# Kernel tuning notes

Measured on AMD Instinct MI355X. Metric: run time of the kernel, lower is better.

## Reference

```python
import jax, jax.numpy as jnp
import numpy as np

BN_EPS = 1e-3


def _three_nn(unknown, known):
    # unknown: [B, N2, 3] query points; known: [B, N1, 3]
    # returns squared distances and indices of the 3 nearest known points
    # (CUDA three_nn returns squared euclidean distances).
    d2 = (jnp.sum(unknown * unknown, -1)[:, :, None]
          + jnp.sum(known * known, -1)[:, None, :]
          - 2.0 * jnp.einsum('bnd,bmd->bnm', unknown, known))  # [B, N2, N1]
    neg_top, ind = jax.lax.top_k(-d2, 3)                        # [B, N2, 3]
    dist2 = jnp.maximum(-neg_top, 0.0)
    return dist2, ind


def _conv_bn_relu(x, W, b, gamma, beta, mean, var):
    # x: [B, C_in, N]; W: [C_out, C_in] (1x1 conv); inference-mode BN
    y = jnp.einsum('oc,bcn->bon', W, x) + b[None, :, None]
    scale = gamma / jnp.sqrt(var + BN_EPS)
    y = (y - mean[None, :, None]) * scale[None, :, None] + beta[None, :, None]
    return jax.nn.relu(y)


def setup_inputs() -> dict:
    key = jax.random.key(0)
    ks = jax.random.split(key, 12)
    B, N1, N2, C1, C2, H = 2, 4096, 16384, 256, 128, 256
    return {
        'points1': jax.random.normal(ks[0], (B, 3, N1), jnp.float32),
        'points2': jax.random.normal(ks[1], (B, 3, N2), jnp.float32),
        'features1': jax.random.normal(ks[2], (B, C1, N1), jnp.float32),
        'features2': jax.random.normal(ks[3], (B, C2, N2), jnp.float32),
        'W1': jax.random.normal(ks[4], (H, C1 + C2), jnp.float32) * 0.05,
        'b1': jax.random.normal(ks[5], (H,), jnp.float32) * 0.05,
        'gamma1': jnp.ones((H,), jnp.float32),
        'beta1': jnp.zeros((H,), jnp.float32),
        'mean1': jax.random.normal(ks[6], (H,), jnp.float32) * 0.1,
        'var1': jax.random.uniform(ks[7], (H,), jnp.float32, 0.5, 1.5),
        'W2': jax.random.normal(ks[8], (H, H), jnp.float32) * 0.05,
        'b2': jax.random.normal(ks[9], (H,), jnp.float32) * 0.05,
        'gamma2': jnp.ones((H,), jnp.float32),
        'beta2': jnp.zeros((H,), jnp.float32),
        'mean2': jax.random.normal(ks[10], (H,), jnp.float32) * 0.1,
        'var2': jax.random.uniform(ks[11], (H,), jnp.float32, 0.5, 1.5),
    }


def reference(points1, points2, features1, features2,
              W1, b1, gamma1, beta1, mean1, var1,
              W2, b2, gamma2, beta2, mean2, var2):
    # 3-NN of each dense point (points2) among coarse points (points1)
    unknown = jnp.swapaxes(points2, 1, 2)  # [B, N2, 3]
    known = jnp.swapaxes(points1, 1, 2)    # [B, N1, 3]
    dist, ind = _three_nn(unknown, known)  # dist: squared distances [B, N2, 3]
    dist = dist * dist                     # forward squares again (as in source)
    dist = jnp.maximum(dist, 1e-10)
    inv = 1.0 / dist
    weights = inv / jnp.sum(inv, axis=2, keepdims=True)  # [B, N2, 3]

    # gather features of the 3 neighbors: features1 [B, C1, N1] -> [B, N2, 3, C1]
    f1 = jnp.swapaxes(features1, 1, 2)  # [B, N1, C1]
    gathered = jax.vmap(lambda f, i: f[i])(f1, ind)  # [B, N2, 3, C1]
    interp = jnp.einsum('bnkc,bnk->bcn', gathered, weights)  # [B, C1, N2]

    x = jnp.concatenate([interp, features2], axis=1)  # [B, C1+C2, N2]
    x = _conv_bn_relu(x, W1, b1, gamma1, beta1, mean1, var1)
    x = _conv_bn_relu(x, W2, b2, gamma2, beta2, mean2, var2)
    return x
```

## Files before the change

### kernel.cpp

```cpp
#include <hip/hip_runtime.h>
#include <cstdint>
#include <cstddef>

#define N1 4096
#define N2 16384
#define C1 256
#define C2 128
#define HH 256
#define K1 384
#define BQ 32768
#define KPAD 392
#define NCH 16

typedef float  f32x4  __attribute__((ext_vector_type(4)));
typedef __bf16 bf16x8 __attribute__((ext_vector_type(8)));
typedef __bf16 bf16x4 __attribute__((ext_vector_type(4)));

__device__ __forceinline__ float exact_dd(float ux, float uy, float uz,
                                          float su, float4 p) {
  float dot = __fadd_rn(__fadd_rn(__fmul_rn(ux, p.x), __fmul_rn(uy, p.y)),
                        __fmul_rn(uz, p.z));
  return __builtin_fmaf(dot, -2.0f, __fadd_rn(su, p.w));
}

#define LEXINS(da, db, dc, ia, ib, ic, dd, jj)                                 \
  {                                                                            \
    bool ca = ((dd) < (da)) || ((dd) == (da) && (jj) < (ia));                  \
    bool cb = ((dd) < (db)) || ((dd) == (db) && (jj) < (ib));                  \
    bool cc = ((dd) < (dc)) || ((dd) == (dc) && (jj) < (ic));                  \
    dc = cb ? (db) : (cc ? (dd) : (dc));                                       \
    ic = cb ? (ib) : (cc ? (jj) : (ic));                                       \
    db = ca ? (da) : (cb ? (dd) : (db));                                       \
    ib = ca ? (ia) : (cb ? (jj) : (ib));                                       \
    da = ca ? (dd) : (da);                                                     \
    ia = ca ? (jj) : (ia);                                                     \
  }

#define KMIN4(K1_, K2_, K3_, K4_, x)                                           \
  {                                                                            \
    float n1 = fminf((K1_), (x));                                              \
    float n2 = __builtin_amdgcn_fmed3f((K1_), (x), (K2_));                     \
    float n3 = __builtin_amdgcn_fmed3f((K2_), (x), (K3_));                     \
    float n4 = __builtin_amdgcn_fmed3f((K3_), (x), (K4_));                     \
    K1_ = n1; K2_ = n2; K3_ = n3; K4_ = n4;                                    \
  }

#define POINTQ(ux, uy, uz, su, px, py, pz, pw, jj, Ka, Kb, Kc, Kd)             \
  {                                                                            \
    float dot_ = __fadd_rn(                                                    \
        __fadd_rn(__fmul_rn((ux), (px)), __fmul_rn((uy), (py))),               \
        __fmul_rn((uz), (pz)));                                                \
    float dd_ = __builtin_fmaf(dot_, -2.0f, __fadd_rn((su), (pw)));            \
    float xk_ = __uint_as_float((__float_as_uint(dd_) & 0xFFFFF000u) |         \
                                ((unsigned)(jj) & 0x00000FFFu));               \
    KMIN4(Ka, Kb, Kc, Kd, xk_);                                                \
  }

__global__ __launch_bounds__(256) void k_prep(
    const float* __restrict__ p1,
    const float* __restrict__ W1, const float* __restrict__ W2,
    const float* __restrict__ b1, const float* __restrict__ g1,
    const float* __restrict__ be1, const float* __restrict__ mm1,
    const float* __restrict__ vv1,
    const float* __restrict__ b2, const float* __restrict__ g2,
    const float* __restrict__ be2, const float* __restrict__ mm2,
    const float* __restrict__ vv2,
    float* __restrict__ pts8, float4* __restrict__ pts4,
    __bf16* __restrict__ W1b, __bf16* __restrict__ W2b,
    float* __restrict__ scsh) {
  int idx = blockIdx.x * 256 + threadIdx.x;
  if (idx < HH * K1) W1b[idx] = (__bf16)W1[idx];
  if (idx < HH * HH) W2b[idx] = (__bf16)W2[idx];
  if (idx < 2 * N1) {
    int b = idx >> 12, j = idx & (N1 - 1);
    const float* p = p1 + (size_t)b * 3 * N1;
    float x = p[j], y = p[N1 + j], z = p[2 * N1 + j];
    float sk = __fadd_rn(__fadd_rn(__fmul_rn(x, x), __fmul_rn(y, y)),
                         __fmul_rn(z, z));
    size_t base = ((size_t)b * (N1 / 2) + (j >> 1)) * 8 + (j & 1);
    pts8[base + 0] = x;
    pts8[base + 2] = y;
    pts8[base + 4] = z;
    pts8[base + 6] = sk;
    pts4[idx] = make_float4(x, y, z, sk);
  }
  if (idx < HH) {
    float sc = g1[idx] / sqrtf(vv1[idx] + 1e-3f);
    scsh[idx]          = sc;
    scsh[HH + idx]     = fmaf(b1[idx] - mm1[idx], sc, be1[idx]);
    float s2 = g2[idx] / sqrtf(vv2[idx] + 1e-3f);
    scsh[2 * HH + idx] = s2;
    scsh[3 * HH + idx] = fmaf(b2[idx] - mm2[idx], s2, be2[idx]);
  }
}

__global__ __launch_bounds__(256) void k_nn(
    const float* __restrict__ p2, const float4* __restrict__ pts8v,
    float* __restrict__ keybuf) {
#pragma clang fp contract(off)
  __shared__ float4 spts[256];
  const int bx = blockIdx.x;
  const int ch = bx & (NCH - 1);
  const int qt = bx >> 4;
  const int b  = qt >> 5;
  const int nA = ((qt & 31) << 9) + threadIdx.x;
  const int nB = nA + 256;

  {
    const float4* g = pts8v + (size_t)b * 4096 + ch * 256;
    spts[threadIdx.x] = g[threadIdx.x];
  }

  const float* p2b = p2 + (size_t)b * 3 * N2;
  float uxA = p2b[nA], uyA = p2b[N2 + nA], uzA = p2b[2 * N2 + nA];
  float suA = __fadd_rn(__fadd_rn(__fmul_rn(uxA, uxA), __fmul_rn(uyA, uyA)),
                        __fmul_rn(uzA, uzA));
  float uxB = p2b[nB], uyB = p2b[N2 + nB], uzB = p2b[2 * N2 + nB];
  float suB = __fadd_rn(__fadd_rn(__fmul_rn(uxB, uxB), __fmul_rn(uyB, uyB)),
                        __fmul_rn(uzB, uzB));
  __syncthreads();

  const int j0 = ch * 256;
  float KaA = 3.0e38f, KbA = 3.0e38f, KcA = 3.0e38f, KdA = 3.0e38f;
  float KaB = 3.0e38f, KbB = 3.0e38f, KcB = 3.0e38f, KdB = 3.0e38f;
#pragma unroll 4
  for (int k = 0; k < 128; ++k) {
    float4 q0 = spts[2 * k];
    float4 q1 = spts[2 * k + 1];
    int i0 = j0 + 2 * k;
    int i1 = j0 + 2 * k + 1;
    POINTQ(uxA, uyA, uzA, suA, q0.x, q0.z, q1.x, q1.z, i0, KaA, KbA, KcA, KdA);
    POINTQ(uxA, uyA, uzA, suA, q0.y, q0.w, q1.y, q1.w, i1, KaA, KbA, KcA, KdA);
    POINTQ(uxB, uyB, uzB, suB, q0.x, q0.z, q1.x, q1.z, i0, KaB, KbB, KcB, KdB);
    POINTQ(uxB, uyB, uzB, suB, q0.y, q0.w, q1.y, q1.w, i1, KaB, KbB, KcB, KdB);
  }

  int qA = b * N2 + nA;
  int qB = b * N2 + nB;
  keybuf[(ch * 4 + 0) * BQ + qA] = KaA;
  keybuf[(ch * 4 + 1) * BQ + qA] = KbA;
  keybuf[(ch * 4 + 2) * BQ + qA] = KcA;
  keybuf[(ch * 4 + 3) * BQ + qA] = KdA;
  keybuf[(ch * 4 + 0) * BQ + qB] = KaB;
  keybuf[(ch * 4 + 1) * BQ + qB] = KbB;
  keybuf[(ch * 4 + 2) * BQ + qB] = KcB;
  keybuf[(ch * 4 + 3) * BQ + qB] = KdB;
}

__global__ __launch_bounds__(256) void k_merge(
    const float* __restrict__ keybuf, const float4* __restrict__ pts4,
    const float* __restrict__ p2,
    float* __restrict__ wbuf, int* __restrict__ ibuf) {
#pragma clang fp contract(off)
  int tid = blockIdx.x * 256 + threadIdx.x;
  int sub = tid & 3;
  int q = tid >> 2;
  int b = q >> 14, n = q & (N2 - 1);

  const float* p2b = p2 + (size_t)b * 3 * N2;
  float ux = p2b[n], uy = p2b[N2 + n], uz = p2b[2 * N2 + n];
  float su = __fadd_rn(__fadd_rn(__fmul_rn(ux, ux), __fmul_rn(uy, uy)),
                       __fmul_rn(uz, uz));

  float Ka = 3.0e38f, Kb = 3.0e38f, Kc = 3.0e38f, Kd = 3.0e38f;
#pragma unroll 4
  for (int m = 0; m < 16; ++m) {
    float x = keybuf[(sub * 16 + m) * BQ + q];
    KMIN4(Ka, Kb, Kc, Kd, x);
  }
#pragma unroll
  for (int msk = 1; msk <= 2; msk <<= 1) {
    float ea = __shfl_xor(Ka, msk, 64), eb = __shfl_xor(Kb, msk, 64);
    float ec = __shfl_xor(Kc, msk, 64), ed = __shfl_xor(Kd, msk, 64);
    KMIN4(Ka, Kb, Kc, Kd, ea);
    KMIN4(Ka, Kb, Kc, Kd, eb);
    KMIN4(Ka, Kb, Kc, Kd, ec);
    KMIN4(Ka, Kb, Kc, Kd, ed);
  }
  if (sub != 0) return;

  bool flag = (__float_as_uint(Kc) >> 12) == (__float_as_uint(Kd) >> 12);
  const float4* pb = pts4 + (size_t)b * N1;
  float da, db, dc;
  int ia, ib, ic;
  if (!flag) {
    ia = (int)(__float_as_uint(Ka) & 0xFFFu);
    ib = (int)(__float_as_uint(Kb) & 0xFFFu);
    ic = (int)(__float_as_uint(Kc) & 0xFFFu);
    da = exact_dd(ux, uy, uz, su, pb[ia]);
    db = exact_dd(ux, uy, uz, su, pb[ib]);
    dc = exact_dd(ux, uy, uz, su, pb[ic]);
  } else {
    da = 3.0e38f; db = 3.0e38f; dc = 3.0e38f;
    ia = 0x7fffffff; ib = 0x7fffffff; ic = 0x7fffffff;
    for (int i = 0; i < 4 * NCH; ++i) {
      float x = keybuf[i * BQ + q];
      int jj = (int)(__float_as_uint(x) & 0xFFFu);
      float dd = exact_dd(ux, uy, uz, su, pb[jj]);
      LEXINS(da, db, dc, ia, ib, ic, dd, jj);
    }
  }

  float qa = fmaxf(da, 0.0f), qb = fmaxf(db, 0.0f), qc = fmaxf(dc, 0.0f);
  qa = fmaxf(__fmul_rn(qa, qa), 1e-10f);
  qb = fmaxf(__fmul_rn(qb, qb), 1e-10f);
  qc = fmaxf(__fmul_rn(qc, qc), 1e-10f);
  float va = __fdiv_rn(1.0f, qa);
  float vb = __fdiv_rn(1.0f, qb);
  float vc = __fdiv_rn(1.0f, qc);
  float s = __fadd_rn(__fadd_rn(va, vb), vc);
  wbuf[q]           = __fdiv_rn(va, s);
  wbuf[BQ + q]      = __fdiv_rn(vb, s);
  wbuf[2 * BQ + q]  = __fdiv_rn(vc, s);
  ibuf[q]          = ia;
  ibuf[BQ + q]     = ib;
  ibuf[2 * BQ + q] = ic;
}

__global__ __launch_bounds__(256) void k_transpose(
    const float* __restrict__ f1, float* __restrict__ f1T) {
  __shared__ float tile[64][65];
  const int bx = blockIdx.x;
  const int b = bx >> 8;
  const int rest = bx & 255;
  const int ct = rest >> 6;
  const int ntb = (rest & 63) << 6;
  const int t = threadIdx.x;
  const int ln = t & 63, g = t >> 6;

  const float* src = f1 + ((size_t)b * C1 + ct * 64) * N1 + ntb;
  for (int k = 0; k < 16; ++k) {
    int c = (k << 2) + g;
    tile[c][ln] = src[(size_t)c * N1 + ln];
  }
  __syncthreads();
  float* dst = f1T + ((size_t)b * N1 + ntb) * C1 + ct * 64;
  for (int k = 0; k < 16; ++k) {
    int nn = (k << 2) + g;
    dst[(size_t)nn * C1 + ln] = tile[ln][nn];
  }
}

__global__ __launch_bounds__(512) void k_fused(
    const float* __restrict__ f1T, const float* __restrict__ f2,
    const float* __restrict__ wbuf, const int* __restrict__ ibuf,
    const __bf16* __restrict__ W1b, const __bf16* __restrict__ W2b,
    const float* __restrict__ scsh, float* __restrict__ out) {
  __shared__ __bf16 sX[64 * KPAD];
  const int t = threadIdx.x;
  const int bx = blockIdx.x;
  const int b = bx >> 8;
  const int n0 = (bx & 255) << 6;

  {
    const int nn = t >> 3, qq = t & 7;
    const int gi = b * N2 + n0 + nn;
    const float w0 = wbuf[gi], w1 = wbuf[BQ + gi], w2 = wbuf[2 * BQ + gi];
    const int i0 = ibuf[gi], i1 = ibuf[BQ + gi], i2 = ibuf[2 * BQ + gi];
    const float4* r0 = (const float4*)(f1T + ((size_t)b * N1 + i0) * C1);
    const float4* r1 = (const float4*)(f1T + ((size_t)b * N1 + i1) * C1);
    const float4* r2 = (const float4*)(f1T + ((size_t)b * N1 + i2) * C1);
#pragma unroll 4
    for (int m = 0; m < 8; ++m) {
      int idx4 = (qq << 3) + m;
      float4 a = r0[idx4], c4 = r1[idx4], d4 = r2[idx4];
      bf16x4 v;
      v[0] = (__bf16)fmaf(w0, a.x, fmaf(w1, c4.x, w2 * d4.x));
      v[1] = (__bf16)fmaf(w0, a.y, fmaf(w1, c4.y, w2 * d4.y));
      v[2] = (__bf16)fmaf(w0, a.z, fmaf(w1, c4.z, w2 * d4.z));
      v[3] = (__bf16)fmaf(w0, a.w, fmaf(w1, c4.w, w2 * d4.w));
      *(bf16x4*)&sX[nn * KPAD + (idx4 << 2)] = v;
    }
  }
  {
    const int col = t & 63, g = t >> 6;
    const float* f2b = f2 + (size_t)b * C2 * N2 + n0 + col;
#pragma unroll
    for (int m = 0; m < 4; ++m) {
      int c4 = (g << 4) + (m << 2);
      bf16x4 v;
      v[0] = (__bf16)f2b[(size_t)(c4 + 0) * N2];
      v[1] = (__bf16)f2b[(size_t)(c4 + 1) * N2];
      v[2] = (__bf16)f2b[(size_t)(c4 + 2) * N2];
      v[3] = (__bf16)f2b[(size_t)(c4 + 3) * N2];
      *(bf16x4*)&sX[col * KPAD + 256 + c4] = v;
    }
  }
  __syncthreads();

  const int l  = t & 63;
  const int wv = __builtin_amdgcn_readfirstlane(t >> 6);
  const int ob = wv << 5;
  const int lm = l & 15, lg = l >> 4;

  f32x4 acc[2][4];
#pragma unroll
  for (int mt = 0; mt < 2; ++mt)
#pragma unroll
    for (int nt = 0; nt < 4; ++nt) acc[mt][nt] = (f32x4)0.0f;

  for (int ks = 0; ks < 12; ++ks) {
    bf16x8 af[2], bfr[4];
#pragma unroll
    for (int mt = 0; mt < 2; ++mt)
      af[mt] = *(const bf16x8*)(W1b + (size_t)(ob + mt * 16 + lm) * K1 +
                                ks * 32 + lg * 8);
#pragma unroll
    for (int nt = 0; nt < 4; ++nt)
      bfr[nt] = *(const bf16x8*)&sX[(nt * 16 + lm) * KPAD + ks * 32 + lg * 8];
#pragma unroll
    for (int mt = 0; mt < 2; ++mt)
#pragma unroll
      for (int nt = 0; nt < 4; ++nt)
        acc[mt][nt] = __builtin_amdgcn_mfma_f32_16x16x32_bf16(
            af[mt], bfr[nt], acc[mt][nt], 0, 0, 0);
  }
  __syncthreads();

#pragma unroll
  for (int mt = 0; mt < 2; ++mt) {
    int rb = ob + mt * 16 + lg * 4;
    float4 sc4 = *(const float4*)(scsh + rb);
    float4 sh4 = *(const float4*)(scsh + HH + rb);
#pragma unroll
    for (int nt = 0; nt < 4; ++nt) {
      int colc = nt * 16 + lm;
      bf16x4 v;
      v[0] = (__bf16)fmaxf(fmaf(acc[mt][nt][0], sc4.x, sh4.x), 0.0f);
      v[1] = (__bf16)fmaxf(fmaf(acc[mt][nt][1], sc4.y, sh4.y), 0.0f);
      v[2] = (__bf16)fmaxf(fmaf(acc[mt][nt][2], sc4.z, sh4.z), 0.0f);
      v[3] = (__bf16)fmaxf(fmaf(acc[mt][nt][3], sc4.w, sh4.w), 0.0f);
      *(bf16x4*)&sX[colc * KPAD + rb] = v;
    }
  }
  __syncthreads();

  f32x4 ac2[2][4];
#pragma unroll
  for (int mt = 0; mt < 2; ++mt)
#pragma unroll
    for (int nt = 0; nt < 4; ++nt) ac2[mt][nt] = (f32x4)0.0f;
  for (int ks = 0; ks < 8; ++ks) {
    bf16x8 af[2], bfr[4];
#pragma unroll
    for (int mt = 0; mt < 2; ++mt)
      af[mt] = *(const bf16x8*)(W2b + (size_t)(ob + mt * 16 + lm) * HH +
                                ks * 32 + lg * 8);
#pragma unroll
    for (int nt = 0; nt < 4; ++nt)
      bfr[nt] = *(const bf16x8*)&sX[(nt * 16 + lm) * KPAD + ks * 32 + lg * 8];
#pragma unroll
    for (int mt = 0; mt < 2; ++mt)
#pragma unroll
      for (int nt = 0; nt < 4; ++nt)
        ac2[mt][nt] = __builtin_amdgcn_mfma_f32_16x16x32_bf16(
            af[mt], bfr[nt], ac2[mt][nt], 0, 0, 0);
  }

  float* outb = out + (size_t)b * HH * N2 + n0;
#pragma unroll
  for (int mt = 0; mt < 2; ++mt) {
    int rb = ob + mt * 16 + lg * 4;
    float4 sc4 = *(const float4*)(scsh + 2 * HH + rb);
    float4 sh4 = *(const float4*)(scsh + 3 * HH + rb);
#pragma unroll
    for (int nt = 0; nt < 4; ++nt) {
      int colc = nt * 16 + lm;
      outb[(size_t)(rb + 0) * N2 + colc] =
          fmaxf(fmaf(ac2[mt][nt][0], sc4.x, sh4.x), 0.0f);
      outb[(size_t)(rb + 1) * N2 + colc] =
          fmaxf(fmaf(ac2[mt][nt][1], sc4.y, sh4.y), 0.0f);
      outb[(size_t)(rb + 2) * N2 + colc] =
          fmaxf(fmaf(ac2[mt][nt][2], sc4.z, sh4.z), 0.0f);
      outb[(size_t)(rb + 3) * N2 + colc] =
          fmaxf(fmaf(ac2[mt][nt][3], sc4.w, sh4.w), 0.0f);
    }
  }
}

extern "C" void kernel_launch(void* const* d_in, const int* in_sizes, int n_in,
                              void* d_out, int out_size, void* d_ws, size_t ws_size,
                              hipStream_t stream) {
  const float* p1  = (const float*)d_in[0];
  const float* p2  = (const float*)d_in[1];
  const float* f1  = (const float*)d_in[2];
  const float* f2  = (const float*)d_in[3];
  const float* W1  = (const float*)d_in[4];
  const float* bb1 = (const float*)d_in[5];
  const float* g1  = (const float*)d_in[6];
  const float* be1 = (const float*)d_in[7];
  const float* mm1 = (const float*)d_in[8];
  const float* vv1 = (const float*)d_in[9];
  const float* W2  = (const float*)d_in[10];
  const float* bb2 = (const float*)d_in[11];
  const float* g2  = (const float*)d_in[12];
  const float* be2 = (const float*)d_in[13];
  const float* mm2 = (const float*)d_in[14];
  const float* vv2 = (const float*)d_in[15];
  float* out = (float*)d_out;

  char* ws = (char*)d_ws;
  float*  keybuf = (float*)(ws);
  float*  f1T    = (float*)(ws);
  float*  wbuf   = (float*)(ws + 8388608);
  int*    ibuf   = (int*)  (ws + 8781824);
  float*  pts8   = (float*)(ws + 9175040);
  float4* pts4   = (float4*)(ws + 9306112);
  __bf16* W1b    = (__bf16*)(ws + 9437184);
  __bf16* W2b    = (__bf16*)(ws + 9633792);
  float*  scsh   = (float*)(ws + 9764864);

  k_prep<<<384, 256, 0, stream>>>(p1, W1, W2,
                                  bb1, g1, be1, mm1, vv1,
                                  bb2, g2, be2, mm2, vv2,
                                  pts8, pts4, W1b, W2b, scsh);
  k_nn<<<1024, 256, 0, stream>>>(p2, (const float4*)pts8, keybuf);
  k_merge<<<512, 256, 0, stream>>>(keybuf, pts4, p2, wbuf, ibuf);
  k_transpose<<<512, 256, 0, stream>>>(f1, f1T);
  k_fused<<<512, 512, 0, stream>>>(f1T, f2, wbuf, ibuf, W1b, W2b, scsh, out);
}
```

Baseline: 122.1 us.

## Fuse nearest-neighbour search and merge into one kernel with 8-lane query split

Replaces the two-pass 3-NN search (chunked partial top-4 written to a key buffer, then a merge kernel) with one kernel. In it, 8 lanes share each query, each scans a strided eighth of the known points straight from global memory, and the lanes combine results with shuffles. This drops the key buffer write and read and one launch. In exchange it loses the shared-memory tile, so every lane reads all 4096 points from global/L2, and each thread now handles only one query instead of two, which lowers per-thread reuse.

After: 231.3 us. 89.4% more time.

```diff
diff --git a/kernel.cpp b/kernel.cpp
--- a/kernel.cpp
+++ b/kernel.cpp
@@ -10,7 +10,6 @@
 #define K1 384
 #define BQ 32768
 #define KPAD 392
-#define NCH 16
 
 typedef float  f32x4  __attribute__((ext_vector_type(4)));
 typedef __bf16 bf16x8 __attribute__((ext_vector_type(8)));
@@ -65,7 +64,7 @@
     const float* __restrict__ b2, const float* __restrict__ g2,
     const float* __restrict__ be2, const float* __restrict__ mm2,
     const float* __restrict__ vv2,
-    float* __restrict__ pts8, float4* __restrict__ pts4,
+    float4* __restrict__ pts4,
     __bf16* __restrict__ W1b, __bf16* __restrict__ W2b,
     float* __restrict__ scsh) {
   int idx = blockIdx.x * 256 + threadIdx.x;
@@ -77,11 +76,6 @@
     float x = p[j], y = p[N1 + j], z = p[2 * N1 + j];
     float sk = __fadd_rn(__fadd_rn(__fmul_rn(x, x), __fmul_rn(y, y)),
                          __fmul_rn(z, z));
-    size_t base = ((size_t)b * (N1 / 2) + (j >> 1)) * 8 + (j & 1);
-    pts8[base + 0] = x;
-    pts8[base + 2] = y;
-    pts8[base + 4] = z;
-    pts8[base + 6] = sk;
     pts4[idx] = make_float4(x, y, z, sk);
   }
   if (idx < HH) {
@@ -95,81 +89,31 @@
 }
 
 __global__ __launch_bounds__(256) void k_nn(
-    const float* __restrict__ p2, const float4* __restrict__ pts8v,
-    float* __restrict__ keybuf) {
-#pragma clang fp contract(off)
-  __shared__ float4 spts[256];
-  const int bx = blockIdx.x;
-  const int ch = bx & (NCH - 1);
-  const int qt = bx >> 4;
-  const int b  = qt >> 5;
-  const int nA = ((qt & 31) << 9) + threadIdx.x;
-  const int nB = nA + 256;
-
-  {
-    const float4* g = pts8v + (size_t)b * 4096 + ch * 256;
-    spts[threadIdx.x] = g[threadIdx.x];
-  }
-
-  const float* p2b = p2 + (size_t)b * 3 * N2;
-  float uxA = p2b[nA], uyA = p2b[N2 + nA], uzA = p2b[2 * N2 + nA];
-  float suA = __fadd_rn(__fadd_rn(__fmul_rn(uxA, uxA), __fmul_rn(uyA, uyA)),
-                        __fmul_rn(uzA, uzA));
-  float uxB = p2b[nB], uyB = p2b[N2 + nB], uzB = p2b[2 * N2 + nB];
-  float suB = __fadd_rn(__fadd_rn(__fmul_rn(uxB, uxB), __fmul_rn(uyB, uyB)),
-                        __fmul_rn(uzB, uzB));
-  __syncthreads();
-
-  const int j0 = ch * 256;
-  float KaA = 3.0e38f, KbA = 3.0e38f, KcA = 3.0e38f, KdA = 3.0e38f;
-  float KaB = 3.0e38f, KbB = 3.0e38f, KcB = 3.0e38f, KdB = 3.0e38f;
-#pragma unroll 4
-  for (int k = 0; k < 128; ++k) {
-    float4 q0 = spts[2 * k];
-    float4 q1 = spts[2 * k + 1];
-    int i0 = j0 + 2 * k;
-    int i1 = j0 + 2 * k + 1;
-    POINTQ(uxA, uyA, uzA, suA, q0.x, q0.z, q1.x, q1.z, i0, KaA, KbA, KcA, KdA);
-    POINTQ(uxA, uyA, uzA, suA, q0.y, q0.w, q1.y, q1.w, i1, KaA, KbA, KcA, KdA);
-    POINTQ(uxB, uyB, uzB, suB, q0.x, q0.z, q1.x, q1.z, i0, KaB, KbB, KcB, KdB);
-    POINTQ(uxB, uyB, uzB, suB, q0.y, q0.w, q1.y, q1.w, i1, KaB, KbB, KcB, KdB);
-  }
-
-  int qA = b * N2 + nA;
-  int qB = b * N2 + nB;
-  keybuf[(ch * 4 + 0) * BQ + qA] = KaA;
-  keybuf[(ch * 4 + 1) * BQ + qA] = KbA;
-  keybuf[(ch * 4 + 2) * BQ + qA] = KcA;
-  keybuf[(ch * 4 + 3) * BQ + qA] = KdA;
-  keybuf[(ch * 4 + 0) * BQ + qB] = KaB;
-  keybuf[(ch * 4 + 1) * BQ + qB] = KbB;
-  keybuf[(ch * 4 + 2) * BQ + qB] = KcB;
-  keybuf[(ch * 4 + 3) * BQ + qB] = KdB;
-}
-
-__global__ __launch_bounds__(256) void k_merge(
-    const float* __restrict__ keybuf, const float4* __restrict__ pts4,
-    const float* __restrict__ p2,
+    const float* __restrict__ p2, const float4* __restrict__ pts4,
     float* __restrict__ wbuf, int* __restrict__ ibuf) {
 #pragma clang fp contract(off)
-  int tid = blockIdx.x * 256 + threadIdx.x;
-  int sub = tid & 3;
-  int q = tid >> 2;
-  int b = q >> 14, n = q & (N2 - 1);
+  const int t = threadIdx.x;
+  const int sub = t & 7;
+  const int qi = blockIdx.x * 32 + (t >> 3);
+  const int b  = qi >> 14;
+  const int n  = qi & (N2 - 1);
 
   const float* p2b = p2 + (size_t)b * 3 * N2;
   float ux = p2b[n], uy = p2b[N2 + n], uz = p2b[2 * N2 + n];
   float su = __fadd_rn(__fadd_rn(__fmul_rn(ux, ux), __fmul_rn(uy, uy)),
                        __fmul_rn(uz, uz));
 
+  const float4* pb = pts4 + (size_t)b * N1;
   float Ka = 3.0e38f, Kb = 3.0e38f, Kc = 3.0e38f, Kd = 3.0e38f;
-#pragma unroll 4
-  for (int m = 0; m < 16; ++m) {
-    float x = keybuf[(sub * 16 + m) * BQ + q];
-    KMIN4(Ka, Kb, Kc, Kd, x);
-  }
-#pragma unroll
-  for (int msk = 1; msk <= 2; msk <<= 1) {
+#pragma unroll 8
+  for (int k = 0; k < 512; ++k) {
+    int j = (k << 3) + sub;
+    float4 p = pb[j];
+    POINTQ(ux, uy, uz, su, p.x, p.y, p.z, p.w, j, Ka, Kb, Kc, Kd);
+  }
+
+#pragma unroll
+  for (int msk = 1; msk <= 4; msk <<= 1) {
     float ea = __shfl_xor(Ka, msk, 64), eb = __shfl_xor(Kb, msk, 64);
     float ec = __shfl_xor(Kc, msk, 64), ed = __shfl_xor(Kd, msk, 64);
     KMIN4(Ka, Kb, Kc, Kd, ea);
@@ -177,44 +121,53 @@
     KMIN4(Ka, Kb, Kc, Kd, ec);
     KMIN4(Ka, Kb, Kc, Kd, ed);
   }
-  if (sub != 0) return;
-
   bool flag = (__float_as_uint(Kc) >> 12) == (__float_as_uint(Kd) >> 12);
-  const float4* pb = pts4 + (size_t)b * N1;
-  float da, db, dc;
-  int ia, ib, ic;
-  if (!flag) {
-    ia = (int)(__float_as_uint(Ka) & 0xFFFu);
-    ib = (int)(__float_as_uint(Kb) & 0xFFFu);
-    ic = (int)(__float_as_uint(Kc) & 0xFFFu);
-    da = exact_dd(ux, uy, uz, su, pb[ia]);
-    db = exact_dd(ux, uy, uz, su, pb[ib]);
-    dc = exact_dd(ux, uy, uz, su, pb[ic]);
-  } else {
-    da = 3.0e38f; db = 3.0e38f; dc = 3.0e38f;
-    ia = 0x7fffffff; ib = 0x7fffffff; ic = 0x7fffffff;
-    for (int i = 0; i < 4 * NCH; ++i) {
-      float x = keybuf[i * BQ + q];
-      int jj = (int)(__float_as_uint(x) & 0xFFFu);
-      float dd = exact_dd(ux, uy, uz, su, pb[jj]);
-      LEXINS(da, db, dc, ia, ib, ic, dd, jj);
-    }
-  }
-
-  float qa = fmaxf(da, 0.0f), qb = fmaxf(db, 0.0f), qc = fmaxf(dc, 0.0f);
-  qa = fmaxf(__fmul_rn(qa, qa), 1e-10f);
-  qb = fmaxf(__fmul_rn(qb, qb), 1e-10f);
-  qc = fmaxf(__fmul_rn(qc, qc), 1e-10f);
-  float va = __fdiv_rn(1.0f, qa);
-  float vb = __fdiv_rn(1.0f, qb);
-  float vc = __fdiv_rn(1.0f, qc);
-  float s = __fadd_rn(__fadd_rn(va, vb), vc);
-  wbuf[q]           = __fdiv_rn(va, s);
-  wbuf[BQ + q]      = __fdiv_rn(vb, s);
-  wbuf[2 * BQ + q]  = __fdiv_rn(vc, s);
-  ibuf[q]          = ia;
-  ibuf[BQ + q]     = ib;
-  ibuf[2 * BQ + q] = ic;
+
+  float da = 3.0e38f, db = 3.0e38f, dc = 3.0e38f;
+  int ia = 0x7fffffff, ib = 0x7fffffff, ic = 0x7fffffff;
+  if (flag) {
+    for (int k = 0; k < 512; ++k) {
+      int j = (k << 3) + sub;
+      float4 p = pb[j];
+      float dd = exact_dd(ux, uy, uz, su, p);
+      LEXINS(da, db, dc, ia, ib, ic, dd, j);
+    }
+#pragma unroll
+    for (int msk = 1; msk <= 4; msk <<= 1) {
+      float ea = __shfl_xor(da, msk, 64), eb = __shfl_xor(db, msk, 64),
+            ec = __shfl_xor(dc, msk, 64);
+      int ja = __shfl_xor(ia, msk, 64), jb = __shfl_xor(ib, msk, 64),
+          jc = __shfl_xor(ic, msk, 64);
+      LEXINS(da, db, dc, ia, ib, ic, ea, ja);
+      LEXINS(da, db, dc, ia, ib, ic, eb, jb);
+      LEXINS(da, db, dc, ia, ib, ic, ec, jc);
+    }
+  }
+
+  if (sub == 0) {
+    if (!flag) {
+      ia = (int)(__float_as_uint(Ka) & 0xFFFu);
+      ib = (int)(__float_as_uint(Kb) & 0xFFFu);
+      ic = (int)(__float_as_uint(Kc) & 0xFFFu);
+      da = exact_dd(ux, uy, uz, su, pb[ia]);
+      db = exact_dd(ux, uy, uz, su, pb[ib]);
+      dc = exact_dd(ux, uy, uz, su, pb[ic]);
+    }
+    float qa = fmaxf(da, 0.0f), qb = fmaxf(db, 0.0f), qc = fmaxf(dc, 0.0f);
+    qa = fmaxf(__fmul_rn(qa, qa), 1e-10f);
+    qb = fmaxf(__fmul_rn(qb, qb), 1e-10f);
+    qc = fmaxf(__fmul_rn(qc, qc), 1e-10f);
+    float va = __fdiv_rn(1.0f, qa);
+    float vb = __fdiv_rn(1.0f, qb);
+    float vc = __fdiv_rn(1.0f, qc);
+    float s = __fadd_rn(__fadd_rn(va, vb), vc);
+    wbuf[qi]          = __fdiv_rn(va, s);
+    wbuf[BQ + qi]     = __fdiv_rn(vb, s);
+    wbuf[2 * BQ + qi] = __fdiv_rn(vc, s);
+    ibuf[qi]          = ia;
+    ibuf[BQ + qi]     = ib;
+    ibuf[2 * BQ + qi] = ic;
+  }
 }
 
 __global__ __launch_bounds__(256) void k_transpose(
@@ -400,22 +353,19 @@
   float* out = (float*)d_out;
 
   char* ws = (char*)d_ws;
-  float*  keybuf = (float*)(ws);
-  float*  f1T    = (float*)(ws);
-  float*  wbuf   = (float*)(ws + 8388608);
-  int*    ibuf   = (int*)  (ws + 8781824);
-  float*  pts8   = (float*)(ws + 9175040);
-  float4* pts4   = (float4*)(ws + 9306112);
-  __bf16* W1b    = (__bf16*)(ws + 9437184);
-  __bf16* W2b    = (__bf16*)(ws + 9633792);
-  float*  scsh   = (float*)(ws + 9764864);
+  float*  f1T  = (float*)(ws);
+  float*  wbuf = (float*)(ws + 8388608);
+  int*    ibuf = (int*)  (ws + 8781824);
+  float4* pts4 = (float4*)(ws + 9175040);
+  __bf16* W1b  = (__bf16*)(ws + 9306112);
+  __bf16* W2b  = (__bf16*)(ws + 9502720);
+  float*  scsh = (float*)(ws + 9633792);
 
   k_prep<<<384, 256, 0, stream>>>(p1, W1, W2,
                                   bb1, g1, be1, mm1, vv1,
                                   bb2, g2, be2, mm2, vv2,
-                                  pts8, pts4, W1b, W2b, scsh);
-  k_nn<<<1024, 256, 0, stream>>>(p2, (const float4*)pts8, keybuf);
-  k_merge<<<512, 256, 0, stream>>>(keybuf, pts4, p2, wbuf, ibuf);
+                                  pts4, W1b, W2b, scsh);
+  k_nn<<<1024, 256, 0, stream>>>(p2, pts4, wbuf, ibuf);
   k_transpose<<<512, 256, 0, stream>>>(f1, f1T);
   k_fused<<<512, 512, 0, stream>>>(f1T, f2, wbuf, ibuf, W1b, W2b, scsh, out);
 }
```
